# Optimization experiments

Hardware: AMD Instinct MI355X
Metric: run time of the kernel (lower is better)

Reference implementation:

```python
import jax, jax.numpy as jnp
import numpy as np

T, B, N, GH, GW, ENC, H, D, TH = 16, 512, 8192, 3, 13, 128, 4, 32, 64
G = GH * GW          # 39 social grid cells
EMB = H * D          # 128 = n_head * att_out
SCALE = 1.0 / np.sqrt(ENC).astype(np.float32)
LN_EPS = 1e-5


def lstm(x, Wih, Whh, bih, bhh):
    # x: [T, Batch, in] -> hidden states [T, Batch, ENC]; torch gate order i,f,g,o
    n = x.shape[1]
    h0 = jnp.zeros((n, ENC), x.dtype)

    def step(carry, xt):
        h, c = carry
        g = xt @ Wih.T + bih + h @ Whh.T + bhh
        i, f, gg, o = jnp.split(g, 4, axis=-1)
        c = jax.nn.sigmoid(f) * c + jax.nn.sigmoid(i) * jnp.tanh(gg)
        h = jax.nn.sigmoid(o) * jnp.tanh(c)
        return (h, c), h

    _, hs = jax.lax.scan(step, (h0, h0), x)
    return hs


def glu(x, Wa, ba, Wg, bg):
    return (x @ Wa.T + ba) * jax.nn.sigmoid(x @ Wg.T + bg)


def layer_norm(x, g, b):
    m = jnp.mean(x, -1, keepdims=True)
    v = jnp.var(x, -1, keepdims=True)
    return (x - m) * jax.lax.rsqrt(v + LN_EPS) * g + b


def setup_inputs():
    key = jax.random.key(0)
    ks = jax.random.split(key, 40)

    def rn(i, sh, s=1.0):
        return jax.random.normal(ks[i], sh, jnp.float32) * s

    inp = {
        'hist': rn(0, (T, B, 2)), 'nbrs': rn(1, (T, N, 2)),
        'va': rn(2, (T, B, 2)), 'nbrsva': rn(3, (T, N, 2)),
        'lane': jnp.zeros((T, B, 1), jnp.float32),
        'nbrslane': jnp.zeros((T, N, 1), jnp.float32),
        'cls': rn(4, (T, B, 1)), 'nbrscls': rn(5, (T, N, 1)),
    }
    # boolean social-grid mask with exactly N true cells (cell-level, full enc dim)
    rng = np.random.default_rng(0)
    flat = np.zeros(B * G, bool)
    flat[rng.permutation(B * G)[:N]] = True
    inp['mask'] = jnp.asarray(np.broadcast_to(flat.reshape(B, GH, GW, 1), (B, GH, GW, ENC)))

    s = 0.05
    inp.update({
        'W1': rn(6, (TH, 5), s), 'b1': jnp.zeros((TH,), jnp.float32),
        'Wih': rn(7, (4 * ENC, TH), s), 'Whh': rn(8, (4 * ENC, ENC), s),
        'bih': jnp.zeros((4 * ENC,), jnp.float32), 'bhh': jnp.zeros((4 * ENC,), jnp.float32),
        'Wq': rn(9, (EMB, ENC), s), 'bq': jnp.zeros((EMB,), jnp.float32),
        'Wk': rn(10, (EMB, ENC), s), 'bk': jnp.zeros((EMB,), jnp.float32),
        'Wv': rn(11, (EMB, ENC), s), 'bv': jnp.zeros((EMB,), jnp.float32),
        'Wg1a': rn(12, (ENC, EMB), s), 'bg1a': jnp.zeros((ENC,), jnp.float32),
        'Wg1g': rn(13, (ENC, EMB), s), 'bg1g': jnp.zeros((ENC,), jnp.float32),
        'Wqt': rn(14, (EMB, ENC), s), 'bqt': jnp.zeros((EMB,), jnp.float32),
        'Wkt': rn(15, (EMB, ENC), s), 'bkt': jnp.zeros((EMB,), jnp.float32),
        'Wvt': rn(16, (EMB, ENC), s), 'bvt': jnp.zeros((EMB,), jnp.float32),
        'Wg2a': rn(17, (ENC, EMB), s), 'bg2a': jnp.zeros((ENC,), jnp.float32),
        'Wg2g': rn(18, (ENC, EMB), s), 'bg2g': jnp.zeros((ENC,), jnp.float32),
        'ln_g': jnp.ones((ENC,), jnp.float32), 'ln_b': jnp.zeros((ENC,), jnp.float32),
    })
    return inp


def reference(hist, nbrs, mask, va, nbrsva, lane, nbrslane, cls, nbrscls,
              W1, b1, Wih, Whh, bih, bhh, Wq, bq, Wk, bk, Wv, bv,
              Wg1a, bg1a, Wg1g, bg1g, Wqt, bqt, Wkt, bkt, Wvt, bvt,
              Wg2a, bg2a, Wg2g, bg2g, ln_g, ln_b):
    # f_length == 5 branch
    hist_in = jnp.concatenate((hist, cls, va), -1)        # [T,B,5]
    nbrs_in = jnp.concatenate((nbrs, nbrscls, nbrsva), -1)  # [T,N,5]

    hist_enc = jax.nn.elu(hist_in @ W1.T + b1)
    hist_h = lstm(hist_enc, Wih, Whh, bih, bhh)           # [T,B,ENC]
    hist_hidden = jnp.transpose(hist_h, (1, 0, 2))        # [B,T,ENC]

    nbrs_enc = jax.nn.elu(nbrs_in @ W1.T + b1)
    nbrs_h = lstm(nbrs_enc, Wih, Whh, bih, bhh)           # [T,N,ENC]

    # masked_scatter: fill true grid cells (row-major over B*G) with neighbor states
    cell = mask[:, :, :, 0].reshape(B * G)                # [B*G] bool
    idx = jnp.cumsum(cell.astype(jnp.int32)) - 1          # position among true cells
    gathered = nbrs_h[:, jnp.clip(idx, 0, N - 1), :]      # [T,B*G,ENC]
    soc = jnp.where(cell[None, :, None], gathered, 0.0).reshape(T, B, G, ENC)

    # spatial multi-head attention (each timestep attends over its own grid)
    q = (hist_hidden @ Wq.T + bq).reshape(B, T, H, D)
    k = (soc @ Wk.T + bk).reshape(T, B, G, H, D)
    v = (soc @ Wv.T + bv).reshape(T, B, G, H, D)
    a = jax.nn.softmax(jnp.einsum('bthd,tbghd->bthg', q, k) * SCALE, -1)
    spa = jnp.einsum('bthg,tbghd->bthd', a, v).reshape(B, T, EMB)
    spa = glu(spa, Wg1a, bg1a, Wg1g, bg1g)

    values = layer_norm(hist_hidden + spa, ln_g, ln_b)    # [B,T,ENC]

    # temporal multi-head attention over T
    qt = (values @ Wqt.T + bqt).reshape(B, T, H, D)
    kt = (values @ Wkt.T + bkt).reshape(B, T, H, D)
    vt = (values @ Wvt.T + bvt).reshape(B, T, H, D)
    at = jax.nn.softmax(jnp.einsum('bthd,bshd->bhts', qt, kt) * SCALE, -1)
    tmp = jnp.einsum('bhts,bshd->bthd', at, vt).reshape(B, T, EMB)
    tmp = glu(tmp, Wg2a, bg2a, Wg2g, bg2g)

    # use_spatial=True
    return layer_norm(hist_hidden + spa + tmp, ln_g, ln_b)
```

## Files before the change

### kernel.cpp

```cpp
#include <hip/hip_runtime.h>
#include <math.h>

#define T_ 16
#define B_ 512
#define N_ 8192
#define G_ 39
#define ENC_ 128
#define TH_ 64
#define MROWS 8704
#define GATE 512
#define KCAT 192
#define SCALE_ 0.08838834764831845f
#define LNEPS 1e-5f
#define NBLK2 272

typedef short bf16x8 __attribute__((ext_vector_type(8)));
typedef float f32x4  __attribute__((ext_vector_type(4)));

__device__ __forceinline__ float sigm(float x){ return 1.0f/(1.0f+expf(-x)); }
__device__ __forceinline__ float rcpf(float x){ return __builtin_amdgcn_rcpf(x); }
__device__ __forceinline__ float sigm_f(float x){ return rcpf(1.0f + __expf(-x)); }
__device__ __forceinline__ float tanh_f(float x){ return 1.0f - 2.0f*rcpf(__expf(2.0f*x) + 1.0f); }
__device__ __forceinline__ unsigned short f2bf(float f){
  unsigned int u = __float_as_uint(f);
  unsigned int r = u + 0x7FFFu + ((u>>16)&1u);
  return (unsigned short)(r>>16);
}
__device__ __forceinline__ float bf2f(unsigned short h){
  return __uint_as_float(((unsigned int)h)<<16);
}

__global__ __launch_bounds__(256) void k_prep(
    const float* __restrict__ Wih, const float* __restrict__ Whh,
    const float* __restrict__ bih, const float* __restrict__ bhh,
    const float* __restrict__ Wk,  const float* __restrict__ bk,
    const float* __restrict__ Wv,  const float* __restrict__ bv,
    const float* __restrict__ Wq,
    const float* __restrict__ Wqt, const float* __restrict__ bqt,
    const float* __restrict__ Wkt, const float* __restrict__ bkt,
    const float* __restrict__ Wvt, const float* __restrict__ bvt,
    const float* __restrict__ Wg1a, const float* __restrict__ bg1a,
    const float* __restrict__ Wg1g, const float* __restrict__ bg1g,
    const float* __restrict__ Wg2a, const float* __restrict__ bg2a,
    const float* __restrict__ Wg2g, const float* __restrict__ bg2g,
    unsigned short* __restrict__ WcatB, float* __restrict__ biasg,
    unsigned short* __restrict__ WkvB,  float* __restrict__ bkv,
    unsigned short* __restrict__ WqB,
    unsigned short* __restrict__ WqktB, float* __restrict__ bqkt,
    unsigned short* __restrict__ Wg1B,  float* __restrict__ bg1,
    unsigned short* __restrict__ Wg2B,  float* __restrict__ bg2)
{
  int i = blockIdx.x*256 + threadIdx.x;
  if (i < GATE*KCAT) {
    int n = i / KCAT, k = i % KCAT;
    WcatB[i] = f2bf((k < TH_) ? Wih[n*TH_ + k] : Whh[n*ENC_ + (k - TH_)]);
  }
  if (i < GATE) biasg[i] = bih[i] + bhh[i];
  if (i < 2*ENC_*ENC_) {
    int n = i >> 7, k = i & 127;
    WkvB[i] = f2bf((n < ENC_) ? Wk[n*ENC_ + k] : Wv[(n-ENC_)*ENC_ + k]);
    Wg1B[i] = f2bf((n < ENC_) ? Wg1a[n*ENC_ + k] : Wg1g[(n-ENC_)*ENC_ + k]);
    Wg2B[i] = f2bf((n < ENC_) ? Wg2a[n*ENC_ + k] : Wg2g[(n-ENC_)*ENC_ + k]);
  }
  if (i < 2*ENC_) {
    bkv[i] = (i < ENC_) ? bk[i] : bv[i-ENC_];
    bg1[i] = (i < ENC_) ? bg1a[i] : bg1g[i-ENC_];
    bg2[i] = (i < ENC_) ? bg2a[i] : bg2g[i-ENC_];
  }
  if (i < ENC_*ENC_) WqB[i] = f2bf(Wq[i]);
  if (i < 3*ENC_*ENC_) {
    int n = i >> 7, k = i & 127;
    float w = (n < ENC_) ? Wqt[n*ENC_ + k] : (n < 2*ENC_) ? Wkt[(n-ENC_)*ENC_ + k]
                                                          : Wvt[(n-2*ENC_)*ENC_ + k];
    WqktB[i] = f2bf(w);
  }
  if (i < 3*ENC_) bqkt[i] = (i < ENC_) ? bqt[i] : (i < 2*ENC_) ? bkt[i-ENC_] : bvt[i-2*ENC_];
}

__device__ __forceinline__ int cellval(const unsigned char* m, long cell, int w) {
  long byte = cell * 128L * w;
  if (w == 1) return m[byte] != 0;
  if (w == 2) return *(const unsigned short*)(m + byte) != 0;
  if (w == 4) return *(const unsigned int*)(m + byte) != 0;
  return *(const unsigned long long*)(m + byte) != 0ULL;
}
__device__ __forceinline__ int cellconsist(const unsigned char* m, long cell, int w) {
  long byte = cell * 128L * w;
  if (w == 1) { unsigned char v = m[byte];
    for (int j = 1; j < 8; ++j) if (m[byte + j] != v) return 0; return 1; }
  if (w == 2) { unsigned short v = *(const unsigned short*)(m + byte);
    for (int j = 1; j < 8; ++j) if (*(const unsigned short*)(m + byte + 2L*j) != v) return 0; return 1; }
  if (w == 4) { unsigned int v = *(const unsigned int*)(m + byte);
    for (int j = 1; j < 8; ++j) if (*(const unsigned int*)(m + byte + 4L*j) != v) return 0; return 1; }
  unsigned long long v = *(const unsigned long long*)(m + byte);
  for (int j = 1; j < 8; ++j) if (*(const unsigned long long*)(m + byte + 8L*j) != v) return 0; return 1;
}

__global__ void k_detect(const unsigned char* __restrict__ mask, int* __restrict__ wsel)
{
  __shared__ int bad;
  int tid = threadIdx.x;
  int chosen = 0;
  for (int w = 1; w <= 8 && !chosen; w <<= 1) {
    if (tid == 0) bad = 0;
    __syncthreads();
    int ok = 1;
    for (int c = tid; c < 512; c += 256) ok &= cellconsist(mask, c, w);
    if (!ok) bad = 1;
    __syncthreads();
    if (!bad) chosen = w;
    __syncthreads();
  }
  if (tid == 0) *wsel = chosen ? chosen : 1;
}

__global__ void k_count(const unsigned char* __restrict__ mask,
                        const int* __restrict__ wsel, int* __restrict__ bcnt)
{
  __shared__ int sc[256];
  int tid = threadIdx.x;
  long cell = (long)blockIdx.x*256 + tid;
  sc[tid] = cellval(mask, cell, *wsel);
  __syncthreads();
  for (int off = 128; off; off >>= 1) {
    if (tid < off) sc[tid] += sc[tid + off];
    __syncthreads();
  }
  if (tid == 0) bcnt[blockIdx.x] = sc[0];
}

__global__ void k_fill(const unsigned char* __restrict__ mask,
                       const int* __restrict__ wsel, const int* __restrict__ bcnt,
                       int* __restrict__ nidx)
{
  __shared__ int sc[256];
  int tid = threadIdx.x, blk = blockIdx.x;
  long cell = (long)blk*256 + tid;
  int on = cellval(mask, cell, *wsel);
  sc[tid] = on;
  __syncthreads();
  for (int off = 1; off < 256; off <<= 1) {
    int v = (tid >= off) ? sc[tid - off] : 0;
    __syncthreads();
    sc[tid] += v;
    __syncthreads();
  }
  int base = 0;
  for (int i = 0; i < blk; ++i) base += bcnt[i];
  nidx[cell] = on ? (base + sc[tid] - 1) : -1;
}

struct AP {
  const float *hist, *cls, *va, *nbrs, *nbrscls, *nbrsva;
  const float *W1, *b1;
  const unsigned short *Wcat, *Wkv, *Wq;
  const float *biasg, *bkv, *bq;
  float *hh;
  float *qbuf;
  unsigned short *knvB;
  unsigned short *Hsp;
  float *csp;
  int c0, tch;
};

__global__ __launch_bounds__(512, 2) void k_lstm(AP p)
{
  __shared__ unsigned short Hl[2*32*128];
  __shared__ unsigned short Xall[16*32*64];

  const int tid = threadIdx.x;
  const int w = tid >> 6, l = tid & 63;
  const int lr = l & 15, lk = (l >> 4) * 8, lq = (l >> 4) * 4;
  const int bi = blockIdx.x, bm = bi * 32;
  const bool ish = (bi < 16);

  bf16x8 wgh[4][4];
  #pragma unroll
  for (int g = 0; g < 4; ++g)
    #pragma unroll
    for (int ks = 0; ks < 4; ++ks)
      wgh[g][ks] = *(const bf16x8*)(p.Wcat + (long)(g*128 + w*16 + lr)*KCAT + 64 + ks*32 + lk);

  const int ch = w*16 + lr;
  const float bgi = p.biasg[ch], bgf = p.biasg[128+ch],
              bgg = p.biasg[256+ch], bgo = p.biasg[384+ch];

  {
    const float w1c0 = p.W1[l*5+0], w1c1 = p.W1[l*5+1], w1c2 = p.W1[l*5+2],
                w1c3 = p.W1[l*5+3], w1c4 = p.W1[l*5+4], b1c = p.b1[l];
    const float* ph = ish ? p.hist : p.nbrs;
    const float* pc = ish ? p.cls  : p.nbrscls;
    const float* pv = ish ? p.va   : p.nbrsva;
    for (int e = w; e < p.tch*32; e += 8) {
      int t4 = e >> 5, row = e & 31;
      long r = ish ? ((long)(p.c0 + t4)*B_ + bm + row)
                   : ((long)(p.c0 + t4)*N_ + (bm - B_) + row);
      float i0 = ph[r*2], i1 = ph[r*2+1], i2 = pc[r], i3 = pv[r*2], i4 = pv[r*2+1];
      float s = b1c + i0*w1c0 + i1*w1c1 + i2*w1c2 + i3*w1c3 + i4*w1c4;
      s = (s > 0.0f) ? s : expm1f(s);
      Xall[(t4*32 + row)*64 + (l ^ ((row & 7) << 3))] = f2bf(s);
    }
  }

  float creg[2][4];
  if (p.c0 == 0) {
    for (int i = tid; i < 32*128; i += 512) Hl[i] = 0;
    #pragma unroll
    for (int mi = 0; mi < 2; ++mi)
      #pragma unroll
      for (int q = 0; q < 4; ++q) creg[mi][q] = 0.0f;
  } else {
    for (int i = tid; i < 32*128; i += 512) Hl[i] = p.Hsp[(long)bm*128 + i];
    #pragma unroll
    for (int mi = 0; mi < 2; ++mi)
      #pragma unroll
      for (int q = 0; q < 4; ++q) creg[mi][q] = p.csp[((long)bi*512 + tid)*8 + mi*4 + q];
  }
  __syncthreads();

  int cur = 0;
  for (int tl = 0; tl < p.tch; ++tl) {
    int t = p.c0 + tl;
    f32x4 acc[4][2] = {};
    #pragma unroll
    for (int ks = 0; ks < 2; ++ks) {
      bf16x8 a[2];
      #pragma unroll
      for (int mi = 0; mi < 2; ++mi) {
        int row = mi*16 + lr;
        int col = (ks*32 + lk) ^ ((row & 7) << 3);
        a[mi] = *(const bf16x8*)(Xall + (tl*32 + row)*64 + col);
      }
      #pragma unroll
      for (int g = 0; g < 4; ++g) {
        bf16x8 b = *(const bf16x8*)(p.Wcat + (long)(g*128 + w*16 + lr)*KCAT + ks*32 + lk);
        #pragma unroll
        for (int mi = 0; mi < 2; ++mi)
          acc[g][mi] = __builtin_amdgcn_mfma_f32_16x16x32_bf16(a[mi], b, acc[g][mi], 0, 0, 0);
      }
    }
    #pragma unroll
    for (int ks = 0; ks < 4; ++ks) {
      bf16x8 a[2];
      #pragma unroll
      for (int mi = 0; mi < 2; ++mi) {
        int row = mi*16 + lr;
        int col = (ks*32 + lk) ^ ((row & 7) << 3);
        a[mi] = *(const bf16x8*)(Hl + cur*4096 + row*128 + col);
      }
      #pragma unroll
      for (int g = 0; g < 4; ++g)
        #pragma unroll
        for (int mi = 0; mi < 2; ++mi)
          acc[g][mi] = __builtin_amdgcn_mfma_f32_16x16x32_bf16(a[mi], wgh[g][ks], acc[g][mi], 0, 0, 0);
    }
    int nxt = cur ^ 1;
    #pragma unroll
    for (int mi = 0; mi < 2; ++mi)
      #pragma unroll
      for (int q = 0; q < 4; ++q) {
        int row = mi*16 + lq + q;
        float gi = acc[0][mi][q] + bgi;
        float gf = acc[1][mi][q] + bgf;
        float gg = acc[2][mi][q] + bgg;
        float go = acc[3][mi][q] + bgo;
        float cc = sigm_f(gf)*creg[mi][q] + sigm_f(gi)*tanh_f(gg);
        creg[mi][q] = cc;
        float hv = sigm_f(go)*tanh_f(cc);
        Hl[nxt*4096 + row*128 + (ch ^ ((row & 7) << 3))] = f2bf(hv);
        if (ish) p.hh[((long)(bm + row)*T_ + t)*128 + ch] = hv;
      }
    __syncthreads();
    cur = nxt;
    if (!ish) {
      f32x4 a2[2][2] = {};
      #pragma unroll
      for (int ks = 0; ks < 4; ++ks) {
        bf16x8 a[2];
        #pragma unroll
        for (int mi = 0; mi < 2; ++mi) {
          int row = mi*16 + lr;
          int col = (ks*32 + lk) ^ ((row & 7) << 3);
          a[mi] = *(const bf16x8*)(Hl + cur*4096 + row*128 + col);
        }
        #pragma unroll
        for (int ni = 0; ni < 2; ++ni) {
          bf16x8 b = *(const bf16x8*)(p.Wkv + (long)(w*32 + ni*16 + lr)*128 + ks*32 + lk);
          #pragma unroll
          for (int mi = 0; mi < 2; ++mi)
            a2[mi][ni] = __builtin_amdgcn_mfma_f32_16x16x32_bf16(a[mi], b, a2[mi][ni], 0, 0, 0);
        }
      }
      long nr = bm - B_;
      #pragma unroll
      for (int mi = 0; mi < 2; ++mi)
        #pragma unroll
        for (int ni = 0; ni < 2; ++ni) {
          int c2 = w*32 + ni*16 + lr;
          float bb = p.bkv[c2];
          #pragma unroll
          for (int q = 0; q < 4; ++q)
            p.knvB[((long)tl*N_ + nr + mi*16 + lq + q)*256 + c2] = f2bf(a2[mi][ni][q] + bb);
        }
    } else {
      f32x4 a2[2] = {};
      #pragma unroll
      for (int ks = 0; ks < 4; ++ks) {
        bf16x8 a[2];
        #pragma unroll
        for (int mi = 0; mi < 2; ++mi) {
          int row = mi*16 + lr;
          int col = (ks*32 + lk) ^ ((row & 7) << 3);
          a[mi] = *(const bf16x8*)(Hl + cur*4096 + row*128 + col);
        }
        bf16x8 b = *(const bf16x8*)(p.Wq + (long)(w*16 + lr)*128 + ks*32 + lk);
        #pragma unroll
        for (int mi = 0; mi < 2; ++mi)
          a2[mi] = __builtin_amdgcn_mfma_f32_16x16x32_bf16(a[mi], b, a2[mi], 0, 0, 0);
      }
      float bb = p.bq[ch];
      #pragma unroll
      for (int mi = 0; mi < 2; ++mi)
        #pragma unroll
        for (int q = 0; q < 4; ++q)
          p.qbuf[((long)t*B_ + bm + mi*16 + lq + q)*128 + ch] = a2[mi][q] + bb;
    }
    __syncthreads();
  }
  for (int i = tid; i < 32*128; i += 512) p.Hsp[(long)bm*128 + i] = Hl[cur*4096 + i];
  #pragma unroll
  for (int mi = 0; mi < 2; ++mi)
    #pragma unroll
    for (int q = 0; q < 4; ++q)
      p.csp[((long)bi*512 + tid)*8 + mi*4 + q] = creg[mi][q];
}

__global__ __launch_bounds__(256) void k_attn_sp(
    int c0, int ltch,
    const float* __restrict__ qbuf, const unsigned short* __restrict__ knvB,
    const float* __restrict__ bk, const float* __restrict__ bv,
    const int* __restrict__ nidx, unsigned short* __restrict__ spaB)
{
  int tid = threadIdx.x;
  int w = tid >> 6, l = tid & 63;
  __shared__ int sn[4][G_];
  __shared__ float aw[4][4][40];
  int gwid = blockIdx.x*4 + w;
  int b = gwid >> ltch;
  int tl = gwid & ((1 << ltch) - 1);
  int t = c0 + tl;
  if (l < G_) sn[w][l] = nidx[b*G_ + l];
  __syncthreads();
  float qA = qbuf[((long)t*B_ + b)*128 + l];
  float qB = qbuf[((long)t*B_ + b)*128 + 64 + l];
  for (int g = 0; g < G_; ++g) {
    int ni = sn[w][g];
    const unsigned short* kr = knvB + ((long)tl*N_ + ni)*256;
    float kA = (ni >= 0) ? bf2f(kr[l])      : bk[l];
    float kB = (ni >= 0) ? bf2f(kr[64 + l]) : bk[64 + l];
    float pA = qA*kA, pB = qB*kB;
    pA += __shfl_xor(pA, 16); pA += __shfl_xor(pA, 8); pA += __shfl_xor(pA, 4);
    pA += __shfl_xor(pA, 2);  pA += __shfl_xor(pA, 1);
    pB += __shfl_xor(pB, 16); pB += __shfl_xor(pB, 8); pB += __shfl_xor(pB, 4);
    pB += __shfl_xor(pB, 2);  pB += __shfl_xor(pB, 1);
    if ((l & 31) == 0) {
      int hb = l >> 5;
      aw[w][hb][g]     = pA * SCALE_;
      aw[w][2+hb][g]   = pB * SCALE_;
    }
  }
  __syncthreads();
  int hA = l >> 5, hB = 2 + (l >> 5);
  float mxA = -1e30f, mxB = -1e30f;
  for (int g = 0; g < G_; ++g) {
    mxA = fmaxf(mxA, aw[w][hA][g]);
    mxB = fmaxf(mxB, aw[w][hB][g]);
  }
  float sA = 0.f, sB = 0.f, oA = 0.f, oB = 0.f;
  for (int g = 0; g < G_; ++g) {
    int ni = sn[w][g];
    const unsigned short* vr = knvB + ((long)tl*N_ + ni)*256 + 128;
    float vA = (ni >= 0) ? bf2f(vr[l])      : bv[l];
    float vB = (ni >= 0) ? bf2f(vr[64 + l]) : bv[64 + l];
    float eA = expf(aw[w][hA][g] - mxA);
    float eB = expf(aw[w][hB][g] - mxB);
    sA += eA; sB += eB; oA += eA*vA; oB += eB*vB;
  }
  spaB[((long)b*T_ + t)*128 + l]      = f2bf(oA / sA);
  spaB[((long)b*T_ + t)*128 + 64 + l] = f2bf(oB / sB);
}

__global__ __launch_bounds__(256) void k_gemm_bf16(
    const unsigned short* __restrict__ A, int lda,
    const unsigned short* __restrict__ W, int ldw,
    const float* __restrict__ bias,
    float* __restrict__ C, int ldc, int K)
{
  int tid = threadIdx.x;
  int w = tid >> 6, l = tid & 63;
  int lr = l & 15, lk = (l >> 4) * 8, lq = (l >> 4) * 4;
  int bm = blockIdx.x * 64;
  int bn = blockIdx.y * 128 + w * 32;
  f32x4 acc[4][2] = {};
  for (int k0 = 0; k0 < K; k0 += 32) {
    bf16x8 a[4], b[2];
    #pragma unroll
    for (int mi = 0; mi < 4; ++mi)
      a[mi] = *(const bf16x8*)(A + (long)(bm + mi*16 + lr)*lda + k0 + lk);
    #pragma unroll
    for (int ni = 0; ni < 2; ++ni)
      b[ni] = *(const bf16x8*)(W + (long)(bn + ni*16 + lr)*ldw + k0 + lk);
    #pragma unroll
    for (int mi = 0; mi < 4; ++mi)
      #pragma unroll
      for (int ni = 0; ni < 2; ++ni)
        acc[mi][ni] = __builtin_amdgcn_mfma_f32_16x16x32_bf16(a[mi], b[ni], acc[mi][ni], 0, 0, 0);
  }
  #pragma unroll
  for (int mi = 0; mi < 4; ++mi)
    #pragma unroll
    for (int ni = 0; ni < 2; ++ni) {
      int col = bn + ni*16 + lr;
      float bb = bias[col];
      #pragma unroll
      for (int q = 0; q < 4; ++q)
        C[(long)(bm + mi*16 + lq + q)*ldc + col] = acc[mi][ni][q] + bb;
    }
}

__global__ __launch_bounds__(256) void k_gemm_bf16o(
    const unsigned short* __restrict__ A, int lda,
    const unsigned short* __restrict__ W, int ldw,
    const float* __restrict__ bias,
    unsigned short* __restrict__ C, int ldc, int K)
{
  int tid = threadIdx.x;
  int w = tid >> 6, l = tid & 63;
  int lr = l & 15, lk = (l >> 4) * 8, lq = (l >> 4) * 4;
  int bm = blockIdx.x * 64;
  int bn = blockIdx.y * 128 + w * 32;
  f32x4 acc[4][2] = {};
  for (int k0 = 0; k0 < K; k0 += 32) {
    bf16x8 a[4], b[2];
    #pragma unroll
    for (int mi = 0; mi < 4; ++mi)
      a[mi] = *(const bf16x8*)(A + (long)(bm + mi*16 + lr)*lda + k0 + lk);
    #pragma unroll
    for (int ni = 0; ni < 2; ++ni)
      b[ni] = *(const bf16x8*)(W + (long)(bn + ni*16 + lr)*ldw + k0 + lk);
    #pragma unroll
    for (int mi = 0; mi < 4; ++mi)
      #pragma unroll
      for (int ni = 0; ni < 2; ++ni)
        acc[mi][ni] = __builtin_amdgcn_mfma_f32_16x16x32_bf16(a[mi], b[ni], acc[mi][ni], 0, 0, 0);
  }
  #pragma unroll
  for (int mi = 0; mi < 4; ++mi)
    #pragma unroll
    for (int ni = 0; ni < 2; ++ni) {
      int col = bn + ni*16 + lr;
      float bb = bias[col];
      #pragma unroll
      for (int q = 0; q < 4; ++q)
        C[(long)(bm + mi*16 + lq + q)*ldc + col] = f2bf(acc[mi][ni][q] + bb);
    }
}

__global__ __launch_bounds__(256) void k_glu_addln(
    const float* __restrict__ t12, const float* __restrict__ res,
    const float* __restrict__ lg, const float* __restrict__ lb,
    float* __restrict__ sum_out, unsigned short* __restrict__ ln_bf16,
    float* __restrict__ ln_f32)
{
  int gtid = blockIdx.x*256 + threadIdx.x;
  int r = gtid >> 6;
  int l = threadIdx.x & 63;
  if (r >= B_*T_) return;
  long b4 = (long)r*256, b2 = (long)r*128;
  float xA = res[b2 + l]      + t12[b4 + l]      * sigm(t12[b4 + 128 + l]);
  float xB = res[b2 + 64 + l] + t12[b4 + 64 + l] * sigm(t12[b4 + 192 + l]);
  if (sum_out) { sum_out[b2 + l] = xA; sum_out[b2 + 64 + l] = xB; }
  float s = xA + xB, s2 = xA*xA + xB*xB;
  #pragma unroll
  for (int off = 32; off; off >>= 1) { s += __shfl_xor(s, off); s2 += __shfl_xor(s2, off); }
  float mean = s * (1.0f/128.0f);
  float var  = s2 * (1.0f/128.0f) - mean*mean;
  float inv  = rsqrtf(var + LNEPS);
  float oA = (xA - mean)*inv*lg[l]      + lb[l];
  float oB = (xB - mean)*inv*lg[64 + l] + lb[64 + l];
  if (ln_bf16) { ln_bf16[b2 + l] = f2bf(oA); ln_bf16[b2 + 64 + l] = f2bf(oB); }
  if (ln_f32)  { ln_f32[b2 + l] = oA;        ln_f32[b2 + 64 + l] = oB; }
}

__global__ __launch_bounds__(128) void k_attn_t(
    const unsigned short* __restrict__ qkt, unsigned short* __restrict__ out)
{
  int b = blockIdx.x, tid = threadIdx.x;
  __shared__ float sq[16][128], sk[16][128], sv[16][128];
  __shared__ float sc[16][4][16];
  for (int i = tid; i < T_*ENC_; i += 128) {
    int tt = i >> 7, j = i & 127;
    long a = ((long)b*T_ + tt)*384;
    sq[tt][j] = bf2f(qkt[a + j]);
    sk[tt][j] = bf2f(qkt[a + 128 + j]);
    sv[tt][j] = bf2f(qkt[a + 256 + j]);
  }
  __syncthreads();
  for (int e = tid; e < 1024; e += 128) {
    int t = e >> 6, s = (e >> 2) & 15, h2 = e & 3;
    float pp = 0.0f;
    #pragma unroll
    for (int d2 = 0; d2 < 32; ++d2) pp += sq[t][h2*32 + d2] * sk[s][h2*32 + d2];
    sc[t][h2][s] = pp * SCALE_;
  }
  __syncthreads();
  if (tid < 64) {
    int t = tid >> 2, h2 = tid & 3;
    float mx = -1e30f;
    for (int s = 0; s < 16; ++s) mx = fmaxf(mx, sc[t][h2][s]);
    float sum = 0.0f;
    for (int s = 0; s < 16; ++s) { float e2 = expf(sc[t][h2][s] - mx); sc[t][h2][s] = e2; sum += e2; }
    float inv = 1.0f / sum;
    for (int s = 0; s < 16; ++s) sc[t][h2][s] *= inv;
  }
  __syncthreads();
  int h2 = tid >> 5, d2 = tid & 31;
  for (int t = 0; t < 16; ++t) {
    float acc = 0.0f;
    for (int s = 0; s < 16; ++s) acc += sc[t][h2][s] * sv[s][h2*32 + d2];
    out[((long)b*T_ + t)*128 + tid] = f2bf(acc);
  }
}

extern "C" void kernel_launch(void* const* d_in, const int* in_sizes, int n_in,
                              void* d_out, int out_size, void* d_ws, size_t ws_size,
                              hipStream_t stream)
{
  const float* hist    = (const float*)d_in[0];
  const float* nbrs    = (const float*)d_in[1];
  const float* va      = (const float*)d_in[2];
  const float* nbrsva  = (const float*)d_in[3];
  const float* cls     = (const float*)d_in[6];
  const float* nbrscls = (const float*)d_in[7];
  const unsigned char* mask = (const unsigned char*)d_in[8];
  const float* W1  = (const float*)d_in[9];
  const float* b1  = (const float*)d_in[10];
  const float* Wih = (const float*)d_in[11];
  const float* Whh = (const float*)d_in[12];
  const float* bih = (const float*)d_in[13];
  const float* bhh = (const float*)d_in[14];
  const float* Wq  = (const float*)d_in[15];
  const float* bq  = (const float*)d_in[16];
  const float* Wk  = (const float*)d_in[17];
  const float* bk  = (const float*)d_in[18];
  const float* Wv  = (const float*)d_in[19];
  const float* bv  = (const float*)d_in[20];
  const float* Wg1a = (const float*)d_in[21];
  const float* bg1a = (const float*)d_in[22];
  const float* Wg1g = (const float*)d_in[23];
  const float* bg1g = (const float*)d_in[24];
  const float* Wqt = (const float*)d_in[25];
  const float* bqt = (const float*)d_in[26];
  const float* Wkt = (const float*)d_in[27];
  const float* bkt = (const float*)d_in[28];
  const float* Wvt = (const float*)d_in[29];
  const float* bvt = (const float*)d_in[30];
  const float* Wg2a = (const float*)d_in[31];
  const float* bg2a = (const float*)d_in[32];
  const float* Wg2g = (const float*)d_in[33];
  const float* bg2g = (const float*)d_in[34];
  const float* ln_g = (const float*)d_in[35];
  const float* ln_b = (const float*)d_in[36];

  size_t fixed = 0;
  {
    size_t items[] = {
      (size_t)GATE*KCAT*2, (size_t)GATE*4, (size_t)2*ENC_*ENC_*2, (size_t)2*ENC_*4,
      (size_t)ENC_*ENC_*2, (size_t)3*ENC_*ENC_*2, (size_t)3*ENC_*4,
      (size_t)2*ENC_*ENC_*2, (size_t)2*ENC_*4, (size_t)2*ENC_*ENC_*2, (size_t)2*ENC_*4,
      (size_t)B_*T_*ENC_*4,
      (size_t)T_*B_*ENC_*4,
      (size_t)MROWS*ENC_*2,
      (size_t)NBLK2*512*8*4,
      (size_t)B_*T_*ENC_*2,
      (size_t)B_*T_*2*ENC_*4,
      (size_t)B_*T_*ENC_*4,
      (size_t)B_*T_*ENC_*2,
      (size_t)B_*T_*3*ENC_*2,
      (size_t)B_*T_*ENC_*2,
      (size_t)B_*G_*4, (size_t)78*4, (size_t)4
    };
    for (size_t v : items) fixed += (v + 255) & ~(size_t)255;
  }
  int tch = 16, ltch = 4;
  while (tch > 2 && fixed + ((size_t)tch*N_*256*2 + 255) > ws_size) { tch >>= 1; ltch--; }

  char* base = (char*)d_ws;
  size_t off = 0;
  auto alloc = [&](size_t bytes) { char* r = base + off; off = (off + bytes + 255) & ~(size_t)255; return r; };
  unsigned short* WcatB = (unsigned short*)alloc(GATE*KCAT*2);
  float*          biasg = (float*)alloc(GATE*4);
  unsigned short* WkvB  = (unsigned short*)alloc(2*ENC_*ENC_*2);
  float*          bkv   = (float*)alloc(2*ENC_*4);
  unsigned short* WqB   = (unsigned short*)alloc(ENC_*ENC_*2);
  unsigned short* WqktB = (unsigned short*)alloc(3*ENC_*ENC_*2);
  float*          bqkt  = (float*)alloc(3*ENC_*4);
  unsigned short* Wg1B  = (unsigned short*)alloc(2*ENC_*ENC_*2);
  float*          bg1   = (float*)alloc(2*ENC_*4);
  unsigned short* Wg2B  = (unsigned short*)alloc(2*ENC_*ENC_*2);
  float*          bg2   = (float*)alloc(2*ENC_*4);
  float*          hh    = (float*)alloc((size_t)B_*T_*ENC_*4);
  float*          qbuf  = (float*)alloc((size_t)T_*B_*ENC_*4);
  unsigned short* Hsp   = (unsigned short*)alloc((size_t)MROWS*ENC_*2);
  float*          csp   = (float*)alloc((size_t)NBLK2*512*8*4);
  unsigned short* spaB  = (unsigned short*)alloc((size_t)B_*T_*ENC_*2);
  float*          t12   = (float*)alloc((size_t)B_*T_*2*ENC_*4);
  float*          S1    = (float*)alloc((size_t)B_*T_*ENC_*4);
  unsigned short* valsB = (unsigned short*)alloc((size_t)B_*T_*ENC_*2);
  unsigned short* qktB  = (unsigned short*)alloc((size_t)B_*T_*3*ENC_*2);
  unsigned short* atoB  = (unsigned short*)alloc((size_t)B_*T_*ENC_*2);
  int*            nidx  = (int*)alloc((size_t)B_*G_*4);
  int*            bcnt  = (int*)alloc(78*4);
  int*            wsel  = (int*)alloc(4);
  unsigned short* knvB  = (unsigned short*)alloc((size_t)tch*N_*256*2);

  k_prep<<<384, 256, 0, stream>>>(
      Wih, Whh, bih, bhh, Wk, bk, Wv, bv, Wq,
      Wqt, bqt, Wkt, bkt, Wvt, bvt,
      Wg1a, bg1a, Wg1g, bg1g, Wg2a, bg2a, Wg2g, bg2g,
      WcatB, biasg, WkvB, bkv, WqB, WqktB, bqkt, Wg1B, bg1, Wg2B, bg2);
  k_detect<<<1, 256, 0, stream>>>(mask, wsel);
  k_count<<<78, 256, 0, stream>>>(mask, wsel, bcnt);
  k_fill<<<78, 256, 0, stream>>>(mask, wsel, bcnt, nidx);

  AP ap;
  ap.hist = hist; ap.cls = cls; ap.va = va;
  ap.nbrs = nbrs; ap.nbrscls = nbrscls; ap.nbrsva = nbrsva;
  ap.W1 = W1; ap.b1 = b1;
  ap.Wcat = WcatB; ap.Wkv = WkvB; ap.Wq = WqB;
  ap.biasg = biasg; ap.bkv = bkv; ap.bq = bq;
  ap.hh = hh; ap.qbuf = qbuf; ap.knvB = knvB; ap.Hsp = Hsp; ap.csp = csp;
  ap.tch = tch;
  for (int c0 = 0; c0 < T_; c0 += tch) {
    ap.c0 = c0;
    k_lstm<<<NBLK2, 512, 0, stream>>>(ap);
    k_attn_sp<<<(B_*tch)/4, 256, 0, stream>>>(c0, ltch, qbuf, knvB, bk, bv, nidx, spaB);
  }

  k_gemm_bf16<<<dim3((B_*T_)/64, 2), 256, 0, stream>>>(spaB, 128, Wg1B, 128, bg1, t12, 256, 128);
  k_glu_addln<<<(B_*T_*64)/256, 256, 0, stream>>>(t12, hh, ln_g, ln_b, S1, valsB, nullptr);
  k_gemm_bf16o<<<dim3((B_*T_)/64, 3), 256, 0, stream>>>(valsB, 128, WqktB, 128, bqkt, qktB, 384, 128);
  k_attn_t<<<B_, 128, 0, stream>>>(qktB, atoB);
  k_gemm_bf16<<<dim3((B_*T_)/64, 2), 256, 0, stream>>>(atoB, 128, Wg2B, 128, bg2, t12, 256, 128);
  k_glu_addln<<<(B_*T_*64)/256, 256, 0, stream>>>(t12, S1, ln_g, ln_b, nullptr, nullptr, (float*)d_out);
}
```

Baseline: 341.3 us.

## Give each wavefront its own 16-row LSTM tile and precompute input encoding

The LSTM kernel is reorganized so each wavefront independently owns 16 batch rows and all 512 gate columns. This removes the block-wide __syncthreads per timestep and cross-wave sharing of the hidden state, using a per-wave padded LDS buffer instead. Gate and projection weights are now streamed from global or L2 on every step rather than held in registers. The input encoder (linear plus ELU) moves to a separate kernel that writes a bf16 buffer for all timesteps. This adds global traffic and an extra launch, and drops occupancy to 136 blocks of 256 threads, which is fewer than the CU count.

```diff
diff --git a/kernel.cpp b/kernel.cpp
--- a/kernel.cpp
+++ b/kernel.cpp
@@ -12,7 +12,7 @@
 #define KCAT 192
 #define SCALE_ 0.08838834764831845f
 #define LNEPS 1e-5f
-#define NBLK2 272
+#define NBLK3 136
 
 typedef short bf16x8 __attribute__((ext_vector_type(8)));
 typedef float f32x4  __attribute__((ext_vector_type(4)));
@@ -150,10 +150,30 @@
   nidx[cell] = on ? (base + sc[tid] - 1) : -1;
 }
 
+__global__ __launch_bounds__(256) void k_encode_all(
+    const float* __restrict__ hist, const float* __restrict__ cls, const float* __restrict__ va,
+    const float* __restrict__ nbrs, const float* __restrict__ nbrscls, const float* __restrict__ nbrsva,
+    const float* __restrict__ W1, const float* __restrict__ b1,
+    unsigned short* __restrict__ XencB)
+{
+  int i = blockIdx.x*256 + threadIdx.x;
+  int t = blockIdx.y;
+  int o = i & 63, m = i >> 6;
+  float in0, in1, in2, in3, in4;
+  if (m < B_) {
+    int r = t*B_ + m;
+    in0 = hist[r*2]; in1 = hist[r*2+1]; in2 = cls[r]; in3 = va[r*2]; in4 = va[r*2+1];
+  } else {
+    int r = t*N_ + (m - B_);
+    in0 = nbrs[r*2]; in1 = nbrs[r*2+1]; in2 = nbrscls[r]; in3 = nbrsva[r*2]; in4 = nbrsva[r*2+1];
+  }
+  const float* w = W1 + o*5;
+  float s = b1[o] + in0*w[0] + in1*w[1] + in2*w[2] + in3*w[3] + in4*w[4];
+  XencB[((long)t*MROWS + m)*64 + o] = f2bf((s > 0.0f) ? s : expm1f(s));
+}
+
 struct AP {
-  const float *hist, *cls, *va, *nbrs, *nbrscls, *nbrsva;
-  const float *W1, *b1;
-  const unsigned short *Wcat, *Wkv, *Wq;
+  const unsigned short *Xenc, *Wcat, *Wkv, *Wq;
   const float *biasg, *bkv, *bq;
   float *hh;
   float *qbuf;
@@ -163,176 +183,132 @@
   int c0, tch;
 };
 
-__global__ __launch_bounds__(512, 2) void k_lstm(AP p)
-{
-  __shared__ unsigned short Hl[2*32*128];
-  __shared__ unsigned short Xall[16*32*64];
-
+__global__ __launch_bounds__(256, 1) void k_lstm(AP p)
+{
+  __shared__ unsigned short Hl[4][16*136 + 8];
   const int tid = threadIdx.x;
   const int w = tid >> 6, l = tid & 63;
   const int lr = l & 15, lk = (l >> 4) * 8, lq = (l >> 4) * 4;
-  const int bi = blockIdx.x, bm = bi * 32;
-  const bool ish = (bi < 16);
-
-  bf16x8 wgh[4][4];
+  const int wgid = blockIdx.x*4 + w;
+  const bool ish = (wgid < 32);
+  const int bm16 = wgid * 16;
+  unsigned short* Hw = &Hl[w][0];
+
+  float bg[4][8];
   #pragma unroll
   for (int g = 0; g < 4; ++g)
     #pragma unroll
-    for (int ks = 0; ks < 4; ++ks)
-      wgh[g][ks] = *(const bf16x8*)(p.Wcat + (long)(g*128 + w*16 + lr)*KCAT + 64 + ks*32 + lk);
-
-  const int ch = w*16 + lr;
-  const float bgi = p.biasg[ch], bgf = p.biasg[128+ch],
-              bgg = p.biasg[256+ch], bgo = p.biasg[384+ch];
-
-  {
-    const float w1c0 = p.W1[l*5+0], w1c1 = p.W1[l*5+1], w1c2 = p.W1[l*5+2],
-                w1c3 = p.W1[l*5+3], w1c4 = p.W1[l*5+4], b1c = p.b1[l];
-    const float* ph = ish ? p.hist : p.nbrs;
-    const float* pc = ish ? p.cls  : p.nbrscls;
-    const float* pv = ish ? p.va   : p.nbrsva;
-    for (int e = w; e < p.tch*32; e += 8) {
-      int t4 = e >> 5, row = e & 31;
-      long r = ish ? ((long)(p.c0 + t4)*B_ + bm + row)
-                   : ((long)(p.c0 + t4)*N_ + (bm - B_) + row);
-      float i0 = ph[r*2], i1 = ph[r*2+1], i2 = pc[r], i3 = pv[r*2], i4 = pv[r*2+1];
-      float s = b1c + i0*w1c0 + i1*w1c1 + i2*w1c2 + i3*w1c3 + i4*w1c4;
-      s = (s > 0.0f) ? s : expm1f(s);
-      Xall[(t4*32 + row)*64 + (l ^ ((row & 7) << 3))] = f2bf(s);
+    for (int cx = 0; cx < 8; ++cx)
+      bg[g][cx] = p.biasg[g*128 + cx*16 + lr];
+  float bpro[16];
+  if (!ish) {
+    #pragma unroll
+    for (int ni = 0; ni < 16; ++ni) bpro[ni] = p.bkv[ni*16 + lr];
+  } else {
+    #pragma unroll
+    for (int ni = 0; ni < 8; ++ni) bpro[ni] = p.bq[ni*16 + lr];
+  }
+
+  float creg[8][4];
+  if (p.c0 == 0) {
+    for (int e = l; e < 16*136; e += 64) Hw[e] = 0;
+    #pragma unroll
+    for (int cx = 0; cx < 8; ++cx)
+      #pragma unroll
+      for (int q = 0; q < 4; ++q) creg[cx][q] = 0.0f;
+  } else {
+    for (int e = l; e < 16*128; e += 64) {
+      int r = e >> 7, c = e & 127;
+      Hw[r*136 + c] = p.Hsp[((long)bm16 + r)*128 + c];
     }
-  }
-
-  float creg[2][4];
-  if (p.c0 == 0) {
-    for (int i = tid; i < 32*128; i += 512) Hl[i] = 0;
-    #pragma unroll
-    for (int mi = 0; mi < 2; ++mi)
-      #pragma unroll
-      for (int q = 0; q < 4; ++q) creg[mi][q] = 0.0f;
-  } else {
-    for (int i = tid; i < 32*128; i += 512) Hl[i] = p.Hsp[(long)bm*128 + i];
-    #pragma unroll
-    for (int mi = 0; mi < 2; ++mi)
-      #pragma unroll
-      for (int q = 0; q < 4; ++q) creg[mi][q] = p.csp[((long)bi*512 + tid)*8 + mi*4 + q];
-  }
-  __syncthreads();
-
-  int cur = 0;
+    #pragma unroll
+    for (int cx = 0; cx < 8; ++cx)
+      #pragma unroll
+      for (int q = 0; q < 4; ++q)
+        creg[cx][q] = p.csp[((long)blockIdx.x*256 + tid)*32 + cx*4 + q];
+  }
+
+  #pragma unroll 1
   for (int tl = 0; tl < p.tch; ++tl) {
     int t = p.c0 + tl;
-    f32x4 acc[4][2] = {};
-    #pragma unroll
-    for (int ks = 0; ks < 2; ++ks) {
-      bf16x8 a[2];
-      #pragma unroll
-      for (int mi = 0; mi < 2; ++mi) {
-        int row = mi*16 + lr;
-        int col = (ks*32 + lk) ^ ((row & 7) << 3);
-        a[mi] = *(const bf16x8*)(Xall + (tl*32 + row)*64 + col);
+    bf16x8 ax[2];
+    #pragma unroll
+    for (int ks = 0; ks < 2; ++ks)
+      ax[ks] = *(const bf16x8*)(p.Xenc + ((long)t*MROWS + bm16 + lr)*64 + ks*32 + lk);
+    bf16x8 ah[4];
+    #pragma unroll
+    for (int ks = 0; ks < 4; ++ks)
+      ah[ks] = *(const bf16x8*)(Hw + lr*136 + ks*32 + lk);
+
+    #pragma unroll
+    for (int cx = 0; cx < 8; ++cx) {
+      f32x4 ac[4] = {};
+      #pragma unroll
+      for (int ks = 0; ks < 6; ++ks) {
+        bf16x8 a = (ks < 2) ? ax[ks] : ah[ks-2];
+        #pragma unroll
+        for (int g = 0; g < 4; ++g) {
+          bf16x8 b = *(const bf16x8*)(p.Wcat + ((long)g*128 + cx*16 + lr)*KCAT + ks*32 + lk);
+          ac[g] = __builtin_amdgcn_mfma_f32_16x16x32_bf16(a, b, ac[g], 0, 0, 0);
+        }
       }
       #pragma unroll
-      for (int g = 0; g < 4; ++g) {
-        bf16x8 b = *(const bf16x8*)(p.Wcat + (long)(g*128 + w*16 + lr)*KCAT + ks*32 + lk);
-        #pragma unroll
-        for (int mi = 0; mi < 2; ++mi)
-          acc[g][mi] = __builtin_amdgcn_mfma_f32_16x16x32_bf16(a[mi], b, acc[g][mi], 0, 0, 0);
+      for (int q = 0; q < 4; ++q) {
+        int row = lq + q;
+        float gi = ac[0][q] + bg[0][cx];
+        float gf = ac[1][q] + bg[1][cx];
+        float gg = ac[2][q] + bg[2][cx];
+        float go = ac[3][q] + bg[3][cx];
+        float cc = sigm_f(gf)*creg[cx][q] + sigm_f(gi)*tanh_f(gg);
+        creg[cx][q] = cc;
+        float hv = sigm_f(go)*tanh_f(cc);
+        Hw[row*136 + cx*16 + lr] = f2bf(hv);
+        if (ish) p.hh[((long)(bm16 + row)*T_ + t)*128 + cx*16 + lr] = hv;
       }
     }
-    #pragma unroll
-    for (int ks = 0; ks < 4; ++ks) {
-      bf16x8 a[2];
-      #pragma unroll
-      for (int mi = 0; mi < 2; ++mi) {
-        int row = mi*16 + lr;
-        int col = (ks*32 + lk) ^ ((row & 7) << 3);
-        a[mi] = *(const bf16x8*)(Hl + cur*4096 + row*128 + col);
-      }
-      #pragma unroll
-      for (int g = 0; g < 4; ++g)
+    bf16x8 an[4];
+    #pragma unroll
+    for (int ks = 0; ks < 4; ++ks)
+      an[ks] = *(const bf16x8*)(Hw + lr*136 + ks*32 + lk);
+    if (!ish) {
+      unsigned short* kvb = p.knvB + ((long)tl*N_ + (bm16 - B_) + lq)*256 + lr;
+      #pragma unroll
+      for (int ni = 0; ni < 16; ++ni) {
+        f32x4 a2 = {};
         #pragma unroll
-        for (int mi = 0; mi < 2; ++mi)
-          acc[g][mi] = __builtin_amdgcn_mfma_f32_16x16x32_bf16(a[mi], wgh[g][ks], acc[g][mi], 0, 0, 0);
-    }
-    int nxt = cur ^ 1;
-    #pragma unroll
-    for (int mi = 0; mi < 2; ++mi)
-      #pragma unroll
-      for (int q = 0; q < 4; ++q) {
-        int row = mi*16 + lq + q;
-        float gi = acc[0][mi][q] + bgi;
-        float gf = acc[1][mi][q] + bgf;
-        float gg = acc[2][mi][q] + bgg;
-        float go = acc[3][mi][q] + bgo;
-        float cc = sigm_f(gf)*creg[mi][q] + sigm_f(gi)*tanh_f(gg);
-        creg[mi][q] = cc;
-        float hv = sigm_f(go)*tanh_f(cc);
-        Hl[nxt*4096 + row*128 + (ch ^ ((row & 7) << 3))] = f2bf(hv);
-        if (ish) p.hh[((long)(bm + row)*T_ + t)*128 + ch] = hv;
-      }
-    __syncthreads();
-    cur = nxt;
-    if (!ish) {
-      f32x4 a2[2][2] = {};
-      #pragma unroll
-      for (int ks = 0; ks < 4; ++ks) {
-        bf16x8 a[2];
-        #pragma unroll
-        for (int mi = 0; mi < 2; ++mi) {
-          int row = mi*16 + lr;
-          int col = (ks*32 + lk) ^ ((row & 7) << 3);
-          a[mi] = *(const bf16x8*)(Hl + cur*4096 + row*128 + col);
+        for (int ks = 0; ks < 4; ++ks) {
+          bf16x8 b = *(const bf16x8*)(p.Wkv + ((long)ni*16 + lr)*128 + ks*32 + lk);
+          a2 = __builtin_amdgcn_mfma_f32_16x16x32_bf16(an[ks], b, a2, 0, 0, 0);
         }
         #pragma unroll
-        for (int ni = 0; ni < 2; ++ni) {
-          bf16x8 b = *(const bf16x8*)(p.Wkv + (long)(w*32 + ni*16 + lr)*128 + ks*32 + lk);
-          #pragma unroll
-          for (int mi = 0; mi < 2; ++mi)
-            a2[mi][ni] = __builtin_amdgcn_mfma_f32_16x16x32_bf16(a[mi], b, a2[mi][ni], 0, 0, 0);
+        for (int q = 0; q < 4; ++q)
+          kvb[q*256 + ni*16] = f2bf(a2[q] + bpro[ni]);
+      }
+    } else {
+      float* qb = p.qbuf + ((long)t*B_ + bm16 + lq)*128 + lr;
+      #pragma unroll
+      for (int ni = 0; ni < 8; ++ni) {
+        f32x4 a2 = {};
+        #pragma unroll
+        for (int ks = 0; ks < 4; ++ks) {
+          bf16x8 b = *(const bf16x8*)(p.Wq + ((long)ni*16 + lr)*128 + ks*32 + lk);
+          a2 = __builtin_amdgcn_mfma_f32_16x16x32_bf16(an[ks], b, a2, 0, 0, 0);
         }
-      }
-      long nr = bm - B_;
-      #pragma unroll
-      for (int mi = 0; mi < 2; ++mi)
-        #pragma unroll
-        for (int ni = 0; ni < 2; ++ni) {
-          int c2 = w*32 + ni*16 + lr;
-          float bb = p.bkv[c2];
-          #pragma unroll
-          for (int q = 0; q < 4; ++q)
-            p.knvB[((long)tl*N_ + nr + mi*16 + lq + q)*256 + c2] = f2bf(a2[mi][ni][q] + bb);
-        }
-    } else {
-      f32x4 a2[2] = {};
-      #pragma unroll
-      for (int ks = 0; ks < 4; ++ks) {
-        bf16x8 a[2];
-        #pragma unroll
-        for (int mi = 0; mi < 2; ++mi) {
-          int row = mi*16 + lr;
-          int col = (ks*32 + lk) ^ ((row & 7) << 3);
-          a[mi] = *(const bf16x8*)(Hl + cur*4096 + row*128 + col);
-        }
-        bf16x8 b = *(const bf16x8*)(p.Wq + (long)(w*16 + lr)*128 + ks*32 + lk);
-        #pragma unroll
-        for (int mi = 0; mi < 2; ++mi)
-          a2[mi] = __builtin_amdgcn_mfma_f32_16x16x32_bf16(a[mi], b, a2[mi], 0, 0, 0);
-      }
-      float bb = p.bq[ch];
-      #pragma unroll
-      for (int mi = 0; mi < 2; ++mi)
         #pragma unroll
         for (int q = 0; q < 4; ++q)
-          p.qbuf[((long)t*B_ + bm + mi*16 + lq + q)*128 + ch] = a2[mi][q] + bb;
+          qb[q*128 + ni*16] = a2[q] + bpro[ni];
+      }
     }
-    __syncthreads();
-  }
-  for (int i = tid; i < 32*128; i += 512) p.Hsp[(long)bm*128 + i] = Hl[cur*4096 + i];
+  }
+  for (int e = l; e < 16*128; e += 64) {
+    int r = e >> 7, c = e & 127;
+    p.Hsp[((long)bm16 + r)*128 + c] = Hw[r*136 + c];
+  }
   #pragma unroll
-  for (int mi = 0; mi < 2; ++mi)
+  for (int cx = 0; cx < 8; ++cx)
     #pragma unroll
     for (int q = 0; q < 4; ++q)
-      p.csp[((long)bi*512 + tid)*8 + mi*4 + q] = creg[mi][q];
+      p.csp[((long)blockIdx.x*256 + tid)*32 + cx*4 + q] = creg[cx][q];
 }
 
 __global__ __launch_bounds__(256) void k_attn_sp(
@@ -578,10 +554,11 @@
       (size_t)GATE*KCAT*2, (size_t)GATE*4, (size_t)2*ENC_*ENC_*2, (size_t)2*ENC_*4,
       (size_t)ENC_*ENC_*2, (size_t)3*ENC_*ENC_*2, (size_t)3*ENC_*4,
       (size_t)2*ENC_*ENC_*2, (size_t)2*ENC_*4, (size_t)2*ENC_*ENC_*2, (size_t)2*ENC_*4,
+      (size_t)T_*MROWS*64*2,
       (size_t)B_*T_*ENC_*4,
       (size_t)T_*B_*ENC_*4,
       (size_t)MROWS*ENC_*2,
-      (size_t)NBLK2*512*8*4,
+      (size_t)NBLK3*256*32*4,
       (size_t)B_*T_*ENC_*2,
       (size_t)B_*T_*2*ENC_*4,
       (size_t)B_*T_*ENC_*4,
@@ -609,10 +586,11 @@
   float*          bg1   = (float*)alloc(2*ENC_*4);
   unsigned short* Wg2B  = (unsigned short*)alloc(2*ENC_*ENC_*2);
   float*          bg2   = (float*)alloc(2*ENC_*4);
+  unsigned short* XencB = (unsigned short*)alloc((size_t)T_*MROWS*64*2);
   float*          hh    = (float*)alloc((size_t)B_*T_*ENC_*4);
   float*          qbuf  = (float*)alloc((size_t)T_*B_*ENC_*4);
   unsigned short* Hsp   = (unsigned short*)alloc((size_t)MROWS*ENC_*2);
-  float*          csp   = (float*)alloc((size_t)NBLK2*512*8*4);
+  float*          csp   = (float*)alloc((size_t)NBLK3*256*32*4);
   unsigned short* spaB  = (unsigned short*)alloc((size_t)B_*T_*ENC_*2);
   float*          t12   = (float*)alloc((size_t)B_*T_*2*ENC_*4);
   float*          S1    = (float*)alloc((size_t)B_*T_*ENC_*4);
@@ -632,18 +610,17 @@
   k_detect<<<1, 256, 0, stream>>>(mask, wsel);
   k_count<<<78, 256, 0, stream>>>(mask, wsel, bcnt);
   k_fill<<<78, 256, 0, stream>>>(mask, wsel, bcnt, nidx);
+  k_encode_all<<<dim3(MROWS*64/256, T_), 256, 0, stream>>>(
+      hist, cls, va, nbrs, nbrscls, nbrsva, W1, b1, XencB);
 
   AP ap;
-  ap.hist = hist; ap.cls = cls; ap.va = va;
-  ap.nbrs = nbrs; ap.nbrscls = nbrscls; ap.nbrsva = nbrsva;
-  ap.W1 = W1; ap.b1 = b1;
-  ap.Wcat = WcatB; ap.Wkv = WkvB; ap.Wq = WqB;
+  ap.Xenc = XencB; ap.Wcat = WcatB; ap.Wkv = WkvB; ap.Wq = WqB;
   ap.biasg = biasg; ap.bkv = bkv; ap.bq = bq;
   ap.hh = hh; ap.qbuf = qbuf; ap.knvB = knvB; ap.Hsp = Hsp; ap.csp = csp;
   ap.tch = tch;
   for (int c0 = 0; c0 < T_; c0 += tch) {
     ap.c0 = c0;
-    k_lstm<<<NBLK2, 512, 0, stream>>>(ap);
+    k_lstm<<<NBLK3, 256, 0, stream>>>(ap);
     k_attn_sp<<<(B_*tch)/4, 256, 0, stream>>>(c0, ltch, qbuf, knvB, bk, bv, nidx, spaB);
   }
 
```

After: 814.3 us. 2.39x slower.
